# Performance work log

Hardware: AMD Instinct MI355X
Metric: run time of the kernel (lower is better)

The kernel has to match this reference:

```python
import jax, jax.numpy as jnp
import numpy as np

N_ITER = 2
M = 0.0
AFF_SOFTMAX = 1.0
BIG = 1e16  # finite sentinel for invalid neighbors (CUDA kernel uses inf)


def _ssn(x, s):
    B, C, H, W = x.shape
    nh, nw = H // s, W // s
    S = nh * nw
    N = H * W
    # append_grid: concat (row, col) coordinate channels scaled by M/stoken
    ii, jj = jnp.meshgrid(jnp.arange(H), jnp.arange(W), indexing='ij')
    grid = jnp.stack([ii, jj], 0).astype(x.dtype) * (M / s)  # (2,H,W)
    xg = jnp.concatenate([x, jnp.broadcast_to(grid[None], (B, 2, H, W))], 1)
    C2 = C + 2
    # adaptive_avg_pool2d with exact divisibility == block mean
    cent = xg.reshape(B, C2, nh, s, nw, s).mean(axis=(3, 5)).reshape(B, C2, S)
    # nearest-neighbor init label map (exact divisibility => i//s)
    ly = jnp.broadcast_to((jnp.arange(H) // s)[:, None], (H, W)).reshape(-1)
    lx = jnp.broadcast_to((jnp.arange(W) // s)[None, :], (H, W)).reshape(-1)
    dy = jnp.repeat(jnp.arange(-1, 2), 3)  # 9-neighborhood offsets
    dx = jnp.tile(jnp.arange(-1, 2), 3)
    ny = ly[None, :] + dy[:, None]  # (9,N)
    nx = lx[None, :] + dx[:, None]
    valid = (ny >= 0) & (ny < nh) & (nx >= 0) & (nx < nw)
    nidx = jnp.clip(ny, 0, nh - 1) * nw + jnp.clip(nx, 0, nw - 1)  # (9,N)
    pix = jnp.arange(N)
    bidx = jnp.arange(B)[:, None, None]
    px = xg.reshape(B, C2, N)
    abs_aff = None
    for k in range(N_ITER):
        cg = cent[:, :, nidx]                              # (B,C2,9,N) gather
        dist = ((px[:, :, None, :] - cg) ** 2).sum(1)      # (B,9,N)
        dist = jnp.where(valid[None], dist, BIG)
        aff = jax.nn.softmax(-AFF_SOFTMAX * dist, axis=1)  # softmax over 9 nbrs
        aff = jnp.where(valid[None], aff, 0.0)
        # sparse_coo_tensor(...).to_dense() == scatter-add into (B,S,N)
        abs_aff = jnp.zeros((B, S, N), x.dtype).at[bidx, nidx[None], pix].add(aff)
        if k < N_ITER - 1:
            num = jnp.einsum('bsn,bcn->bcs', abs_aff, px)  # weighted bmm
            den = abs_aff.sum(2)[:, None] + 1e-16
            cent = num / den
    return abs_aff, S


def setup_inputs() -> dict:
    key = jax.random.key(0)
    x = jax.random.normal(key, (4, 32, 256, 256), dtype=jnp.float32)
    return {"x": x, "stoken_size": 16}


def reference(x, stoken_size):
    return _ssn(x, int(stoken_size))
```

## Files before the change

### kernel.cpp

```cpp
#include <hip/hip_runtime.h>

#define B_  4
#define C_  32
#define H_  256
#define W_  256
#define N_  65536
#define NH_ 16
#define S_  256
#define PADP 260
#define PSTR 304

__device__ __forceinline__ float wave_sum(float v) {
    v += __shfl_down(v, 32);
    v += __shfl_down(v, 16);
    v += __shfl_down(v, 8);
    v += __shfl_down(v, 4);
    v += __shfl_down(v, 2);
    v += __shfl_down(v, 1);
    return v;
}

__device__ __forceinline__ void compute_aff(const float xv[C_], const float (*cl)[C_],
                                            int sy, int sx, float aff[9]) {
    float dist[9];
    #pragma unroll
    for (int k = 0; k < 9; ++k) {
        const int ny = sy + k / 3 - 1, nx = sx + k % 3 - 1;
        const bool valid = (ny >= 0) & (ny < NH_) & (nx >= 0) & (nx < NH_);
        float d = 0.f;
        #pragma unroll
        for (int c = 0; c < C_; ++c) { const float df = xv[c] - cl[k][c]; d += df * df; }
        dist[k] = valid ? d : 1e30f;
    }
    float mind = dist[0];
    #pragma unroll
    for (int k = 1; k < 9; ++k) mind = fminf(mind, dist[k]);
    float sum = 0.f;
    #pragma unroll
    for (int k = 0; k < 9; ++k) {
        const float e = (dist[k] < 1e29f) ? __expf(mind - dist[k]) : 0.f;
        aff[k] = e;
        sum += e;
    }
    const float inv = 1.f / sum;
    #pragma unroll
    for (int k = 0; k < 9; ++k) aff[k] *= inv;
}

__global__ __launch_bounds__(256) void k_cent0(const float* __restrict__ x,
                                               float* __restrict__ cent0) {
    const int blk = blockIdx.x;
    const int b = blk >> 8, s = blk & 255;
    const int sy = s >> 4, sx = s & 15;
    const int t = threadIdx.x;
    const int w = t >> 6, lane = t & 63;
    const int py = sy * 16 + (t >> 4), pxc = sx * 16 + (t & 15);
    const float* xb = x + (size_t)b * C_ * N_ + py * W_ + pxc;
    __shared__ float acc[C_][4];
    #pragma unroll
    for (int c = 0; c < C_; ++c) {
        const float v = wave_sum(xb[c * N_]);
        if (lane == 0) acc[c][w] = v;
    }
    __syncthreads();
    if (t < C_)
        cent0[(size_t)blk * C_ + t] =
            (acc[t][0] + acc[t][1] + acc[t][2] + acc[t][3]) * (1.0f / 256.0f);
}

__global__ __launch_bounds__(256) void k_part(const float* __restrict__ x,
                                              const float* __restrict__ cent0,
                                              float* __restrict__ part) {
    const int blk = blockIdx.x;
    const int b = blk >> 8, s = blk & 255;
    const int sy = s >> 4, sx = s & 15;
    const int t = threadIdx.x;
    const int w = t >> 6, lane = t & 63;
    __shared__ float cl[9][C_];
    __shared__ float xsh[C_][PADP];
    __shared__ float affs[9][256];
    __shared__ float lden[4][9];
    {
        const int k = t >> 5, c = t & 31;
        const int ny = sy + k / 3 - 1, nx = sx + k % 3 - 1;
        const bool valid = (ny >= 0) & (ny < NH_) & (nx >= 0) & (nx < NH_);
        cl[k][c] = valid ? cent0[(size_t)(b * S_ + ny * NH_ + nx) * C_ + c] : 0.f;
    }
    if (t < 32) {
        const int ny = sy + 1, nx = sx + 1;
        const bool valid = (ny < NH_) & (nx < NH_);
        cl[8][t] = valid ? cent0[(size_t)(b * S_ + ny * NH_ + nx) * C_ + t] : 0.f;
    }
    __syncthreads();
    const int py = sy * 16 + (t >> 4), pxc = sx * 16 + (t & 15);
    const float* xb = x + (size_t)b * C_ * N_ + py * W_ + pxc;
    float xv[C_];
    #pragma unroll
    for (int c = 0; c < C_; ++c) { xv[c] = xb[c * N_]; xsh[c][t] = xv[c]; }
    float aff[9];
    compute_aff(xv, cl, sy, sx, aff);
    #pragma unroll
    for (int k = 0; k < 9; ++k) {
        affs[k][t] = aff[k];
        const float v = wave_sum(aff[k]);
        if (lane == 0) lden[w][k] = v;
    }
    __syncthreads();
    {
        const int k = t >> 5, c = t & 31;
        float acc = 0.f;
        #pragma unroll 4
        for (int p = 0; p < 256; p += 4) {
            const float4 a = *(const float4*)&affs[k][p];
            const float4 xc = *(const float4*)&xsh[c][p];
            acc += a.x * xc.x + a.y * xc.y + a.z * xc.z + a.w * xc.w;
        }
        part[(size_t)blk * PSTR + t] = acc;
    }
    if (t < 32) {
        float acc = 0.f;
        #pragma unroll 4
        for (int p = 0; p < 256; p += 4) {
            const float4 a = *(const float4*)&affs[8][p];
            const float4 xc = *(const float4*)&xsh[t][p];
            acc += a.x * xc.x + a.y * xc.y + a.z * xc.z + a.w * xc.w;
        }
        part[(size_t)blk * PSTR + 256 + t] = acc;
    }
    if (t < 9)
        part[(size_t)blk * PSTR + 288 + t] =
            lden[0][t] + lden[1][t] + lden[2][t] + lden[3][t];
}

__global__ __launch_bounds__(256) void k_cent1(const float* __restrict__ part,
                                               float* __restrict__ cent1) {
    const int g = blockIdx.x * 256 + threadIdx.x;
    const int c = g & 31, s = (g >> 5) & 255, b = g >> 13;
    const int sy = s >> 4, sx = s & 15;
    float num = 0.f, den = 0.f;
    #pragma unroll
    for (int k = 0; k < 9; ++k) {
        const int syp = sy - (k / 3 - 1), sxp = sx - (k % 3 - 1);
        if ((syp >= 0) & (syp < NH_) & (sxp >= 0) & (sxp < NH_)) {
            const size_t base = (size_t)(b * S_ + syp * NH_ + sxp) * PSTR;
            num += part[base + k * 32 + c];
            den += part[base + 288 + k];
        }
    }
    cent1[g] = num / (den + 1e-16f);
}

__global__ __launch_bounds__(256) void k_aff9(const float* __restrict__ x,
                                              const float* __restrict__ cent1,
                                              float* __restrict__ aff9) {
    const int blk = blockIdx.x;
    const int b = blk >> 8, s = blk & 255;
    const int sy = s >> 4, sx = s & 15;
    const int t = threadIdx.x;
    __shared__ float cl[9][C_];
    {
        const int k = t >> 5, c = t & 31;
        const int ny = sy + k / 3 - 1, nx = sx + k % 3 - 1;
        const bool valid = (ny >= 0) & (ny < NH_) & (nx >= 0) & (nx < NH_);
        cl[k][c] = valid ? cent1[(size_t)(b * S_ + ny * NH_ + nx) * C_ + c] : 0.f;
    }
    if (t < 32) {
        const int ny = sy + 1, nx = sx + 1;
        const bool valid = (ny < NH_) & (nx < NH_);
        cl[8][t] = valid ? cent1[(size_t)(b * S_ + ny * NH_ + nx) * C_ + t] : 0.f;
    }
    __syncthreads();
    const int py = sy * 16 + (t >> 4), pxc = sx * 16 + (t & 15);
    const int n = py * W_ + pxc;
    const float* xb = x + (size_t)b * C_ * N_ + n;
    float xv[C_];
    #pragma unroll
    for (int c = 0; c < C_; ++c) xv[c] = xb[c * N_];
    float aff[9];
    compute_aff(xv, cl, sy, sx, aff);
    #pragma unroll
    for (int k = 0; k < 9; ++k)
        aff9[(size_t)(b * 9 + k) * N_ + n] = aff[k];
}

__global__ __launch_bounds__(256) void k_write(const float* __restrict__ aff9,
                                               float* __restrict__ out) {
    const unsigned g = blockIdx.x * 256u + threadIdx.x;
    const int b = g >> 22;
    const int s = (g >> 14) & 255;
    const int q = g & 16383;
    const int ly = q >> 10;
    const int lx = (q >> 2) & 15;
    const int dy = (s >> 4) - ly + 1;
    const int dx = (s & 15) - lx + 1;
    float4 v = make_float4(0.f, 0.f, 0.f, 0.f);
    if (((unsigned)dy <= 2u) & ((unsigned)dx <= 2u)) {
        const int k = dy * 3 + dx;
        v = *(const float4*)(aff9 + ((size_t)(b * 9 + k) << 16) + (q << 2));
    }
    ((float4*)out)[g] = v;
    if (g == 0) out[(size_t)B_ * S_ * N_] = 256.0f;
}

extern "C" void kernel_launch(void* const* d_in, const int* in_sizes, int n_in,
                              void* d_out, int out_size, void* d_ws, size_t ws_size,
                              hipStream_t stream) {
    const float* x = (const float*)d_in[0];
    float* ws = (float*)d_ws;
    float* cent0 = ws;
    float* part  = ws + 32768;
    float* cent1 = ws + 32768 + 1024 * PSTR;
    float* aff9  = ws + 32768 + 1024 * PSTR + 32768;
    float* out   = (float*)d_out;

    hipLaunchKernelGGL(k_cent0, dim3(B_ * S_), dim3(256), 0, stream, x, cent0);
    hipLaunchKernelGGL(k_part,  dim3(B_ * S_), dim3(256), 0, stream, x, cent0, part);
    hipLaunchKernelGGL(k_cent1, dim3(B_ * S_ * C_ / 256), dim3(256), 0, stream, part, cent1);
    hipLaunchKernelGGL(k_aff9,  dim3(B_ * S_), dim3(256), 0, stream, x, cent1, aff9);
    hipLaunchKernelGGL(k_write, dim3((B_ * S_ * N_ / 4) / 256), dim3(256), 0, stream,
                       aff9, out);
}
```

Measured before the change: 351.4 us.

## Stage pixel tiles via float4 loads to LDS and coarsen output write kernel

k_part and k_aff9 now load each 16x16 superpixel tile for all 32 channels with float4 global loads into LDS, then read per-thread pixel vectors from shared memory, instead of strided scalar loads. k_aff9 also stages affinities in LDS so that aff9 is written with coalesced float4 stores. The distance loop reads centroids as float4 from LDS, and k_write processes 8 float4 per thread with fewer blocks. The cost is extra LDS use and syncs in k_aff9, which may reduce occupancy. The output write, a 268MB dense store, likely dominates, so gains may be limited.

```diff
diff --git a/kernel.cpp b/kernel.cpp
--- a/kernel.cpp
+++ b/kernel.cpp
@@ -20,6 +20,20 @@
     return v;
 }
 
+__device__ __forceinline__ void stage_tile(const float* __restrict__ x,
+                                           int b, int sy, int sx, int t,
+                                           float (*xsh)[PADP]) {
+    const float* base = x + (size_t)b * C_ * N_ + (sy * 16) * W_ + sx * 16;
+    #pragma unroll
+    for (int i = 0; i < 8; ++i) {
+        const int idx = i * 256 + t;
+        const int c = idx >> 6, p4 = idx & 63;
+        const int py = p4 >> 2, px4 = (p4 & 3) * 4;
+        const float4 v = *(const float4*)(base + (size_t)c * N_ + py * W_ + px4);
+        *(float4*)&xsh[c][p4 * 4] = v;
+    }
+}
+
 __device__ __forceinline__ void compute_aff(const float xv[C_], const float (*cl)[C_],
                                             int sy, int sx, float aff[9]) {
     float dist[9];
@@ -29,7 +43,14 @@
         const bool valid = (ny >= 0) & (ny < NH_) & (nx >= 0) & (nx < NH_);
         float d = 0.f;
         #pragma unroll
-        for (int c = 0; c < C_; ++c) { const float df = xv[c] - cl[k][c]; d += df * df; }
+        for (int c4 = 0; c4 < C_ / 4; ++c4) {
+            const float4 cv = *(const float4*)&cl[k][c4 * 4];
+            const float d0 = xv[c4 * 4 + 0] - cv.x;
+            const float d1 = xv[c4 * 4 + 1] - cv.y;
+            const float d2 = xv[c4 * 4 + 2] - cv.z;
+            const float d3 = xv[c4 * 4 + 3] - cv.w;
+            d += d0 * d0 + d1 * d1 + d2 * d2 + d3 * d3;
+        }
         dist[k] = valid ? d : 1e30f;
     }
     float mind = dist[0];
@@ -45,6 +66,22 @@
     const float inv = 1.f / sum;
     #pragma unroll
     for (int k = 0; k < 9; ++k) aff[k] *= inv;
+}
+
+__device__ __forceinline__ void load_cl(const float* __restrict__ cent,
+                                        int b, int sy, int sx, int t,
+                                        float (*cl)[C_]) {
+    {
+        const int k = t >> 5, c = t & 31;
+        const int ny = sy + k / 3 - 1, nx = sx + k % 3 - 1;
+        const bool valid = (ny >= 0) & (ny < NH_) & (nx >= 0) & (nx < NH_);
+        cl[k][c] = valid ? cent[(size_t)(b * S_ + ny * NH_ + nx) * C_ + c] : 0.f;
+    }
+    if (t < 32) {
+        const int ny = sy + 1, nx = sx + 1;
+        const bool valid = (ny < NH_) & (nx < NH_);
+        cl[8][t] = valid ? cent[(size_t)(b * S_ + ny * NH_ + nx) * C_ + t] : 0.f;
+    }
 }
 
 __global__ __launch_bounds__(256) void k_cent0(const float* __restrict__ x,
@@ -78,25 +115,14 @@
     const int w = t >> 6, lane = t & 63;
     __shared__ float cl[9][C_];
     __shared__ float xsh[C_][PADP];
-    __shared__ float affs[9][256];
+    __shared__ float affs[9][PADP];
     __shared__ float lden[4][9];
-    {
-        const int k = t >> 5, c = t & 31;
-        const int ny = sy + k / 3 - 1, nx = sx + k % 3 - 1;
-        const bool valid = (ny >= 0) & (ny < NH_) & (nx >= 0) & (nx < NH_);
-        cl[k][c] = valid ? cent0[(size_t)(b * S_ + ny * NH_ + nx) * C_ + c] : 0.f;
-    }
-    if (t < 32) {
-        const int ny = sy + 1, nx = sx + 1;
-        const bool valid = (ny < NH_) & (nx < NH_);
-        cl[8][t] = valid ? cent0[(size_t)(b * S_ + ny * NH_ + nx) * C_ + t] : 0.f;
-    }
-    __syncthreads();
-    const int py = sy * 16 + (t >> 4), pxc = sx * 16 + (t & 15);
-    const float* xb = x + (size_t)b * C_ * N_ + py * W_ + pxc;
+    load_cl(cent0, b, sy, sx, t, cl);
+    stage_tile(x, b, sy, sx, t, xsh);
+    __syncthreads();
     float xv[C_];
     #pragma unroll
-    for (int c = 0; c < C_; ++c) { xv[c] = xb[c * N_]; xsh[c][t] = xv[c]; }
+    for (int c = 0; c < C_; ++c) xv[c] = xsh[c][t];
     float aff[9];
     compute_aff(xv, cl, sy, sx, aff);
     #pragma unroll
@@ -108,24 +134,24 @@
     __syncthreads();
     {
         const int k = t >> 5, c = t & 31;
-        float acc = 0.f;
+        float acc2 = 0.f;
         #pragma unroll 4
         for (int p = 0; p < 256; p += 4) {
             const float4 a = *(const float4*)&affs[k][p];
             const float4 xc = *(const float4*)&xsh[c][p];
-            acc += a.x * xc.x + a.y * xc.y + a.z * xc.z + a.w * xc.w;
-        }
-        part[(size_t)blk * PSTR + t] = acc;
+            acc2 += a.x * xc.x + a.y * xc.y + a.z * xc.z + a.w * xc.w;
+        }
+        part[(size_t)blk * PSTR + t] = acc2;
     }
     if (t < 32) {
-        float acc = 0.f;
+        float acc2 = 0.f;
         #pragma unroll 4
         for (int p = 0; p < 256; p += 4) {
             const float4 a = *(const float4*)&affs[8][p];
             const float4 xc = *(const float4*)&xsh[t][p];
-            acc += a.x * xc.x + a.y * xc.y + a.z * xc.z + a.w * xc.w;
-        }
-        part[(size_t)blk * PSTR + 256 + t] = acc;
+            acc2 += a.x * xc.x + a.y * xc.y + a.z * xc.z + a.w * xc.w;
+        }
+        part[(size_t)blk * PSTR + 256 + t] = acc2;
     }
     if (t < 9)
         part[(size_t)blk * PSTR + 288 + t] =
@@ -158,48 +184,53 @@
     const int sy = s >> 4, sx = s & 15;
     const int t = threadIdx.x;
     __shared__ float cl[9][C_];
-    {
-        const int k = t >> 5, c = t & 31;
-        const int ny = sy + k / 3 - 1, nx = sx + k % 3 - 1;
-        const bool valid = (ny >= 0) & (ny < NH_) & (nx >= 0) & (nx < NH_);
-        cl[k][c] = valid ? cent1[(size_t)(b * S_ + ny * NH_ + nx) * C_ + c] : 0.f;
-    }
-    if (t < 32) {
-        const int ny = sy + 1, nx = sx + 1;
-        const bool valid = (ny < NH_) & (nx < NH_);
-        cl[8][t] = valid ? cent1[(size_t)(b * S_ + ny * NH_ + nx) * C_ + t] : 0.f;
-    }
-    __syncthreads();
-    const int py = sy * 16 + (t >> 4), pxc = sx * 16 + (t & 15);
-    const int n = py * W_ + pxc;
-    const float* xb = x + (size_t)b * C_ * N_ + n;
+    __shared__ float xsh[C_][PADP];
+    __shared__ float affs[9][PADP];
+    load_cl(cent1, b, sy, sx, t, cl);
+    stage_tile(x, b, sy, sx, t, xsh);
+    __syncthreads();
     float xv[C_];
     #pragma unroll
-    for (int c = 0; c < C_; ++c) xv[c] = xb[c * N_];
+    for (int c = 0; c < C_; ++c) xv[c] = xsh[c][t];
     float aff[9];
     compute_aff(xv, cl, sy, sx, aff);
     #pragma unroll
-    for (int k = 0; k < 9; ++k)
-        aff9[(size_t)(b * 9 + k) * N_ + n] = aff[k];
+    for (int k = 0; k < 9; ++k) affs[k][t] = aff[k];
+    __syncthreads();
+    #pragma unroll
+    for (int i = 0; i < 3; ++i) {
+        const int idx = i * 256 + t;
+        if (idx < 576) {
+            const int k = idx >> 6, j4 = idx & 63;
+            const int py = j4 >> 2, px4 = (j4 & 3) * 4;
+            const float4 v = *(const float4*)&affs[k][j4 * 4];
+            const int n = (sy * 16 + py) * W_ + sx * 16 + px4;
+            *(float4*)(aff9 + ((size_t)(b * 9 + k) << 16) + n) = v;
+        }
+    }
 }
 
 __global__ __launch_bounds__(256) void k_write(const float* __restrict__ aff9,
                                                float* __restrict__ out) {
-    const unsigned g = blockIdx.x * 256u + threadIdx.x;
-    const int b = g >> 22;
-    const int s = (g >> 14) & 255;
-    const int q = g & 16383;
-    const int ly = q >> 10;
-    const int lx = (q >> 2) & 15;
-    const int dy = (s >> 4) - ly + 1;
-    const int dx = (s & 15) - lx + 1;
-    float4 v = make_float4(0.f, 0.f, 0.f, 0.f);
-    if (((unsigned)dy <= 2u) & ((unsigned)dx <= 2u)) {
-        const int k = dy * 3 + dx;
-        v = *(const float4*)(aff9 + ((size_t)(b * 9 + k) << 16) + (q << 2));
-    }
-    ((float4*)out)[g] = v;
-    if (g == 0) out[(size_t)B_ * S_ * N_] = 256.0f;
+    const int t = threadIdx.x;
+    const int bs = blockIdx.x >> 3;
+    const int b = bs >> 8, s = bs & 255;
+    const int sdy = (s >> 4) + 1, sdx = (s & 15) + 1;
+    const int qb = (blockIdx.x & 7) * 2048 + t;
+    const float* plane = aff9 + ((size_t)b * 9 << 16);
+    float4* outp = (float4*)out + ((size_t)bs << 14);
+    #pragma unroll
+    for (int i = 0; i < 8; ++i) {
+        const int q = qb + i * 256;
+        const int ly = q >> 10;
+        const int lx = (q >> 2) & 15;
+        const int dy = sdy - ly, dx = sdx - lx;
+        float4 v = make_float4(0.f, 0.f, 0.f, 0.f);
+        if (((unsigned)dy <= 2u) & ((unsigned)dx <= 2u))
+            v = *(const float4*)(plane + ((size_t)(dy * 3 + dx) << 16) + (q << 2));
+        outp[q] = v;
+    }
+    if ((blockIdx.x | t) == 0) out[(size_t)B_ * S_ * N_] = 256.0f;
 }
 
 extern "C" void kernel_launch(void* const* d_in, const int* in_sizes, int n_in,
@@ -217,6 +248,5 @@
     hipLaunchKernelGGL(k_part,  dim3(B_ * S_), dim3(256), 0, stream, x, cent0, part);
     hipLaunchKernelGGL(k_cent1, dim3(B_ * S_ * C_ / 256), dim3(256), 0, stream, part, cent1);
     hipLaunchKernelGGL(k_aff9,  dim3(B_ * S_), dim3(256), 0, stream, x, cent1, aff9);
-    hipLaunchKernelGGL(k_write, dim3((B_ * S_ * N_ / 4) / 256), dim3(256), 0, stream,
-                       aff9, out);
-}
+    hipLaunchKernelGGL(k_write, dim3(B_ * S_ * 8), dim3(256), 0, stream, aff9, out);
+}
```

Result: slower. 361.4 us (+2.9%).
